# Kernel optimization log

Hardware: AMD Instinct MI355X
Metric: run time of the kernel (lower is better)

## Reference

```python
import jax, jax.numpy as jnp
import numpy as np

B, N, F = 4096, 64, 128   # batch, max_neighbor, input feature dim
H, D = 8, 64              # num_heads, weight_dims (per head)
HD = H * D


def setup_inputs() -> dict:
    key = jax.random.key(0)
    k1, k2, k3, k4 = jax.random.split(key, 4)
    x = jax.random.normal(k1, (B, N, F), dtype=jnp.float32)
    W_lin = jax.random.normal(k2, (F, HD), dtype=jnp.float32) * (1.0 / np.sqrt(F))
    W_att = jax.random.normal(k3, (2 * HD, H), dtype=jnp.float32) * (1.0 / np.sqrt(2 * HD))
    mask = jax.random.randint(k4, (B, N), 0, 2, dtype=jnp.int32)
    return {"x": x, "W_lin": W_lin, "W_att": W_att, "mask": mask}


def reference(x, W_lin, W_att, mask):
    # dropout is identity (rate 0.0 / inference)
    lin = x @ W_lin                               # [B, N, H*D]
    # src node is neighbor slot 0 of each batch row (the Python-loop gather+tile)
    src = lin[:, 0, :]                            # [B, H*D]
    # attention_layer on concat([src, lin]) == src@W_att[:HD] + lin@W_att[HD:]
    att = src @ W_att[:HD]                        # [B, H]
    att = att[:, None, :] + lin @ W_att[HD:]      # [B, N, H]
    att = jnp.where(att >= 0, att, 0.2 * att)     # LeakyReLU(alpha=0.2)
    aw = jnp.transpose(att, (0, 2, 1))            # [B, H, N]  (split heads + squeeze)
    aw = aw + (mask == 0).astype(jnp.float32)[:, None, :] * (-1e9)
    aw = jax.nn.softmax(aw, axis=2)[..., None]    # [B, H, N, 1]
    lp = jnp.transpose(lin.reshape(B, N, H, D), (0, 2, 1, 3))  # [B, H, N, D]
    weighted = lp * aw                            # [B, H, N, D]
    # fusion 'concat': unstack heads, concat along last -> [B, N, H*D], then ReLU
    out = jnp.transpose(weighted, (0, 2, 1, 3)).reshape(B, N, HD)
    return jax.nn.relu(out)
```

## Files before the change

kernel.cpp:

```cpp
#include <hip/hip_runtime.h>


typedef _Float16 half8  __attribute__((ext_vector_type(8)));
typedef _Float16 half4v __attribute__((ext_vector_type(4)));
typedef float    f32x4  __attribute__((ext_vector_type(4)));

static constexpr int NSEQ  = 64;
static constexpr int FIN   = 128;
static constexpr int HDIM  = 512;
static constexpr int NHEAD = 8;

static constexpr int ATT_OFF    = 34816;
static constexpr int SMEM_BYTES = 39168;

__global__ __launch_bounds__(256) void prep_kernel(const float* __restrict__ wlin,
                                                   const float* __restrict__ watt,
                                                   _Float16* __restrict__ wlinT,
                                                   _Float16* __restrict__ waA)
{
    int t = blockIdx.x * 256 + threadIdx.x;
    if (t < HDIM * FIN) {
        int c = t >> 7;
        int k = t & 127;
        wlinT[t] = (_Float16)wlin[k * HDIM + c];
    }
    if (t < 16 * HDIM) {
        int i     = t & 3;
        int lane  = (t >> 2) & 63;
        int slice = t >> 8;
        int c = (slice >> 2) * 64 + (slice & 3) * 16 + (lane >> 4) * 4 + i;
        int j = lane & 15;
        float v = (j < NHEAD) ? watt[(HDIM + c) * NHEAD + j]
                              : watt[c * NHEAD + (j - NHEAD)];
        waA[t] = (_Float16)v;
    }
}

__global__ __launch_bounds__(512, 4) void fused_kernel(const float* __restrict__ x,
                                                       const _Float16* __restrict__ wlinT,
                                                       const _Float16* __restrict__ waA,
                                                       const int* __restrict__ mask,
                                                       float* __restrict__ out)
{
    __shared__ char smem[SMEM_BYTES] __attribute__((aligned(16)));
    float* attbuf = (float*)smem;
    float* att_s  = (float*)(smem + ATT_OFF);

    const int b    = blockIdx.x;
    const int t    = threadIdx.x;
    const int lane = t & 63;
    const int w    = t >> 6;
    const int l15  = lane & 15;
    const int quad = lane >> 4;

    const int mv = mask[b * NSEQ + lane];

    f32x4 acc[4][4];
    #pragma unroll
    for (int mt = 0; mt < 4; ++mt)
        #pragma unroll
        for (int nt = 0; nt < 4; ++nt)
            acc[mt][nt] = (f32x4){0.f, 0.f, 0.f, 0.f};

    const float* xb = x + (size_t)b * (NSEQ * FIN);
    const int colbase = w * 64;
    #pragma unroll
    for (int ks = 0; ks < 4; ++ks) {
        const int k0 = ks * 32 + quad * 8;
        half8 a[4];
        #pragma unroll
        for (int mt = 0; mt < 4; ++mt)
            a[mt] = *(const half8*)(wlinT + (colbase + mt * 16 + l15) * FIN + k0);
        #pragma unroll
        for (int nt = 0; nt < 4; ++nt) {
            const float* xr = xb + (nt * 16 + l15) * FIN + k0;
            f32x4 v0 = *(const f32x4*)(xr);
            f32x4 v1 = *(const f32x4*)(xr + 4);
            half8 bfr;
            bfr[0] = (_Float16)v0[0]; bfr[1] = (_Float16)v0[1];
            bfr[2] = (_Float16)v0[2]; bfr[3] = (_Float16)v0[3];
            bfr[4] = (_Float16)v1[0]; bfr[5] = (_Float16)v1[1];
            bfr[6] = (_Float16)v1[2]; bfr[7] = (_Float16)v1[3];
            #pragma unroll
            for (int mt = 0; mt < 4; ++mt)
                acc[mt][nt] = __builtin_amdgcn_mfma_f32_16x16x32_f16(a[mt], bfr, acc[mt][nt], 0, 0, 0);
        }
    }

    {
        f32x4 T[4];
        #pragma unroll
        for (int nt = 0; nt < 4; ++nt) T[nt] = (f32x4){0.f, 0.f, 0.f, 0.f};
        #pragma unroll
        for (int mt = 0; mt < 4; ++mt) {
            half4v aF = *(const half4v*)(waA + ((w * 4 + mt) * 64 + lane) * 4);
            #pragma unroll
            for (int nt = 0; nt < 4; ++nt) {
                half4v bF;
                #pragma unroll
                for (int i = 0; i < 4; ++i) bF[i] = (_Float16)acc[mt][nt][i];
                T[nt] = __builtin_amdgcn_mfma_f32_16x16x16f16(aF, bF, T[nt], 0, 0, 0);
            }
        }
        #pragma unroll
        for (int nt = 0; nt < 4; ++nt)
            *(f32x4*)(attbuf + (w * 64 + nt * 16 + l15) * 16 + quad * 4) = T[nt];
    }
    __syncthreads();

    {
        int n  = t >> 3;
        int j0 = (t & 7) * 2;
        float s0 = 0.f, s1 = 0.f;
        #pragma unroll
        for (int ww = 0; ww < 8; ++ww) {
            const float* p = attbuf + (ww * 64 + n) * 16 + j0;
            s0 += p[0]; s1 += p[1];
        }
        att_s[n * 17 + j0]     = s0;
        att_s[n * 17 + j0 + 1] = s1;
    }
    __syncthreads();

    float aw_reg;
    {
        const float pen = (mv == 0) ? -1e9f : 0.0f;
        float a = att_s[lane * 17 + w] + att_s[8 + w];
        a = (a >= 0.0f) ? a : 0.2f * a;
        a += pen;
        float mx = a;
        #pragma unroll
        for (int off = 32; off > 0; off >>= 1)
            mx = fmaxf(mx, __shfl_xor(mx, off, 64));
        float e = __expf(a - mx);
        float s = e;
        #pragma unroll
        for (int off = 32; off > 0; off >>= 1)
            s += __shfl_xor(s, off, 64);
        aw_reg = e / s;
    }

    {
        float* ft = (float*)smem + w * (16 * 68);
        float* outb = out + (size_t)b * (NSEQ * HDIM);
        #pragma unroll
        for (int nt = 0; nt < 4; ++nt) {
            float awv = __shfl(aw_reg, nt * 16 + l15, 64);
            #pragma unroll
            for (int mt = 0; mt < 4; ++mt) {
                f32x4 o;
                #pragma unroll
                for (int i = 0; i < 4; ++i)
                    o[i] = fmaxf(acc[mt][nt][i] * awv, 0.0f);
                *(f32x4*)(ft + l15 * 68 + mt * 16 + quad * 4) = o;
            }
            #pragma unroll
            for (int s = 0; s < 4; ++s) {
                int r = s * 4 + quad;
                f32x4 v = *(const f32x4*)(ft + r * 68 + l15 * 4);
                int n = nt * 16 + r;
                __builtin_nontemporal_store(v, (f32x4*)(outb + n * HDIM + w * 64 + l15 * 4));
            }
        }
    }
}

extern "C" void kernel_launch(void* const* d_in, const int* in_sizes, int n_in,
                              void* d_out, int out_size, void* d_ws, size_t ws_size,
                              hipStream_t stream)
{
    const float* x    = (const float*)d_in[0];
    const float* wlin = (const float*)d_in[1];
    const float* watt = (const float*)d_in[2];
    const int*   mask = (const int*)d_in[3];
    float* out = (float*)d_out;

    _Float16* wlinT = (_Float16*)d_ws;
    _Float16* waA   = wlinT + HDIM * FIN;

    const int B = in_sizes[0] / (NSEQ * FIN);

    prep_kernel<<<256, 256, 0, stream>>>(wlin, watt, wlinT, waA);
    fused_kernel<<<B, 512, 0, stream>>>(x, wlinT, waA, mask, out);
}
```

Before: 746.2 us.

## Process four batches per block with double-buffered async x loads into LDS

Each block now handles four batch rows in sequence. While one row is computed, the next row's x tile is prefetched into a swizzled, double-buffered LDS region using global_load_lds. The cross-wave attention reduction changes from a staged buffer plus a second sync to LDS atomicAdd into a double-buffered accumulator. This aims to hide global load latency and remove one barrier per batch. In exchange LDS use grows to about 70KB per block, which reduces occupancy, and the grid shrinks by four times.

```diff
diff --git a/kernel.cpp b/kernel.cpp
--- a/kernel.cpp
+++ b/kernel.cpp
@@ -5,13 +5,24 @@
 typedef _Float16 half4v __attribute__((ext_vector_type(4)));
 typedef float    f32x4  __attribute__((ext_vector_type(4)));
 
-static constexpr int NSEQ  = 64;
-static constexpr int FIN   = 128;
-static constexpr int HDIM  = 512;
-static constexpr int NHEAD = 8;
-
-static constexpr int ATT_OFF    = 34816;
-static constexpr int SMEM_BYTES = 39168;
+static constexpr int NSEQ   = 64;
+static constexpr int FIN    = 128;
+static constexpr int HDIM   = 512;
+static constexpr int NHEAD  = 8;
+static constexpr int NBATCH = 4;
+static constexpr int AA_LD  = 17;
+
+static constexpr int XS_B       = 32768;
+static constexpr int FT7_OFF    = 65536;
+static constexpr int BLOB_BYTES = 69888;
+
+typedef const __attribute__((address_space(1))) unsigned int* gas_ptr;
+typedef __attribute__((address_space(3))) unsigned int*       las_ptr;
+
+__device__ __forceinline__ void gload_lds16(const void* g, void* l)
+{
+    __builtin_amdgcn_global_load_lds((gas_ptr)g, (las_ptr)l, 16, 0, 0);
+}
 
 __global__ __launch_bounds__(256) void prep_kernel(const float* __restrict__ wlin,
                                                    const float* __restrict__ watt,
@@ -42,126 +53,166 @@
                                                        const int* __restrict__ mask,
                                                        float* __restrict__ out)
 {
-    __shared__ char smem[SMEM_BYTES] __attribute__((aligned(16)));
-    float* attbuf = (float*)smem;
-    float* att_s  = (float*)(smem + ATT_OFF);
-
-    const int b    = blockIdx.x;
+    __shared__ char  smem[BLOB_BYTES] __attribute__((aligned(16)));
+    __shared__ float att_acc_s[2][NSEQ * AA_LD];
+
     const int t    = threadIdx.x;
     const int lane = t & 63;
     const int w    = t >> 6;
     const int l15  = lane & 15;
     const int quad = lane >> 4;
 
-    const int mv = mask[b * NSEQ + lane];
-
-    f32x4 acc[4][4];
-    #pragma unroll
-    for (int mt = 0; mt < 4; ++mt)
+    const int b0 = blockIdx.x * NBATCH;
+
+    {
+        int p0 = t, p1 = t + 512;
+        att_acc_s[0][(p0 >> 4) * AA_LD + (p0 & 15)] = 0.f;
+        att_acc_s[0][(p1 >> 4) * AA_LD + (p1 & 15)] = 0.f;
+        att_acc_s[1][(p0 >> 4) * AA_LD + (p0 & 15)] = 0.f;
+        att_acc_s[1][(p1 >> 4) * AA_LD + (p1 & 15)] = 0.f;
+    }
+
+    {
+        const char* xg = (const char*)(x + (size_t)b0 * (NSEQ * FIN));
         #pragma unroll
-        for (int nt = 0; nt < 4; ++nt)
-            acc[mt][nt] = (f32x4){0.f, 0.f, 0.f, 0.f};
-
-    const float* xb = x + (size_t)b * (NSEQ * FIN);
-    const int colbase = w * 64;
-    #pragma unroll
-    for (int ks = 0; ks < 4; ++ks) {
-        const int k0 = ks * 32 + quad * 8;
-        half8 a[4];
+        for (int j = 0; j < 4; ++j) {
+            int ci = j * 512 + t;
+            int L  = ci * 16;
+            int sw = ((ci >> 5) & 7) << 4;
+            gload_lds16(xg + (L ^ sw), smem + L);
+        }
+    }
+    __syncthreads();
+
+    #pragma unroll 1
+    for (int it = 0; it < NBATCH; ++it) {
+        const int b   = b0 + it;
+        const int cur = it & 1;
+        char*  xc = smem + cur * XS_B;
+        float* aa = att_acc_s[cur];
+
+        if (it + 1 < NBATCH) {
+            const char* xg = (const char*)(x + (size_t)(b + 1) * (NSEQ * FIN));
+            char* xn = smem + (cur ^ 1) * XS_B;
+            #pragma unroll
+            for (int j = 0; j < 4; ++j) {
+                int ci = j * 512 + t;
+                int L  = ci * 16;
+                int sw = ((ci >> 5) & 7) << 4;
+                gload_lds16(xg + (L ^ sw), xn + L);
+            }
+        }
+        const int mv = mask[b * NSEQ + lane];
+
+        f32x4 acc[4][4];
         #pragma unroll
         for (int mt = 0; mt < 4; ++mt)
-            a[mt] = *(const half8*)(wlinT + (colbase + mt * 16 + l15) * FIN + k0);
+            #pragma unroll
+            for (int nt = 0; nt < 4; ++nt)
+                acc[mt][nt] = (f32x4){0.f, 0.f, 0.f, 0.f};
+
+        const int colbase = w * 64;
         #pragma unroll
-        for (int nt = 0; nt < 4; ++nt) {
-            const float* xr = xb + (nt * 16 + l15) * FIN + k0;
-            f32x4 v0 = *(const f32x4*)(xr);
-            f32x4 v1 = *(const f32x4*)(xr + 4);
-            half8 bfr;
-            bfr[0] = (_Float16)v0[0]; bfr[1] = (_Float16)v0[1];
-            bfr[2] = (_Float16)v0[2]; bfr[3] = (_Float16)v0[3];
-            bfr[4] = (_Float16)v1[0]; bfr[5] = (_Float16)v1[1];
-            bfr[6] = (_Float16)v1[2]; bfr[7] = (_Float16)v1[3];
+        for (int ks = 0; ks < 4; ++ks) {
+            const int k0 = ks * 32 + quad * 8;
+            const int cb = k0 * 4;
+            half8 a[4];
             #pragma unroll
             for (int mt = 0; mt < 4; ++mt)
-                acc[mt][nt] = __builtin_amdgcn_mfma_f32_16x16x32_f16(a[mt], bfr, acc[mt][nt], 0, 0, 0);
-        }
-    }
-
-    {
-        f32x4 T[4];
-        #pragma unroll
-        for (int nt = 0; nt < 4; ++nt) T[nt] = (f32x4){0.f, 0.f, 0.f, 0.f};
-        #pragma unroll
-        for (int mt = 0; mt < 4; ++mt) {
-            half4v aF = *(const half4v*)(waA + ((w * 4 + mt) * 64 + lane) * 4);
+                a[mt] = *(const half8*)(wlinT + (colbase + mt * 16 + l15) * FIN + k0);
             #pragma unroll
             for (int nt = 0; nt < 4; ++nt) {
-                half4v bF;
-                #pragma unroll
-                for (int i = 0; i < 4; ++i) bF[i] = (_Float16)acc[mt][nt][i];
-                T[nt] = __builtin_amdgcn_mfma_f32_16x16x16f16(aF, bF, T[nt], 0, 0, 0);
-            }
-        }
-        #pragma unroll
-        for (int nt = 0; nt < 4; ++nt)
-            *(f32x4*)(attbuf + (w * 64 + nt * 16 + l15) * 16 + quad * 4) = T[nt];
-    }
-    __syncthreads();
-
-    {
-        int n  = t >> 3;
-        int j0 = (t & 7) * 2;
-        float s0 = 0.f, s1 = 0.f;
-        #pragma unroll
-        for (int ww = 0; ww < 8; ++ww) {
-            const float* p = attbuf + (ww * 64 + n) * 16 + j0;
-            s0 += p[0]; s1 += p[1];
-        }
-        att_s[n * 17 + j0]     = s0;
-        att_s[n * 17 + j0 + 1] = s1;
-    }
-    __syncthreads();
-
-    float aw_reg;
-    {
-        const float pen = (mv == 0) ? -1e9f : 0.0f;
-        float a = att_s[lane * 17 + w] + att_s[8 + w];
-        a = (a >= 0.0f) ? a : 0.2f * a;
-        a += pen;
-        float mx = a;
-        #pragma unroll
-        for (int off = 32; off > 0; off >>= 1)
-            mx = fmaxf(mx, __shfl_xor(mx, off, 64));
-        float e = __expf(a - mx);
-        float s = e;
-        #pragma unroll
-        for (int off = 32; off > 0; off >>= 1)
-            s += __shfl_xor(s, off, 64);
-        aw_reg = e / s;
-    }
-
-    {
-        float* ft = (float*)smem + w * (16 * 68);
-        float* outb = out + (size_t)b * (NSEQ * HDIM);
-        #pragma unroll
-        for (int nt = 0; nt < 4; ++nt) {
-            float awv = __shfl(aw_reg, nt * 16 + l15, 64);
+                const int n  = nt * 16 + l15;
+                const int sw = (n & 7) << 4;
+                const char* rb = xc + n * 512;
+                f32x4 v0 = *(const f32x4*)(rb + (cb ^ sw));
+                f32x4 v1 = *(const f32x4*)(rb + ((cb + 16) ^ sw));
+                half8 bfr;
+                bfr[0] = (_Float16)v0[0]; bfr[1] = (_Float16)v0[1];
+                bfr[2] = (_Float16)v0[2]; bfr[3] = (_Float16)v0[3];
+                bfr[4] = (_Float16)v1[0]; bfr[5] = (_Float16)v1[1];
+                bfr[6] = (_Float16)v1[2]; bfr[7] = (_Float16)v1[3];
+                #pragma unroll
+                for (int mt = 0; mt < 4; ++mt)
+                    acc[mt][nt] = __builtin_amdgcn_mfma_f32_16x16x32_f16(a[mt], bfr, acc[mt][nt], 0, 0, 0);
+            }
+        }
+
+        {
+            f32x4 T[4];
+            #pragma unroll
+            for (int nt = 0; nt < 4; ++nt) T[nt] = (f32x4){0.f, 0.f, 0.f, 0.f};
             #pragma unroll
             for (int mt = 0; mt < 4; ++mt) {
-                f32x4 o;
+                half4v aF = *(const half4v*)(waA + ((w * 4 + mt) * 64 + lane) * 4);
+                #pragma unroll
+                for (int nt = 0; nt < 4; ++nt) {
+                    half4v bF;
+                    #pragma unroll
+                    for (int i = 0; i < 4; ++i) bF[i] = (_Float16)acc[mt][nt][i];
+                    T[nt] = __builtin_amdgcn_mfma_f32_16x16x16f16(aF, bF, T[nt], 0, 0, 0);
+                }
+            }
+            #pragma unroll
+            for (int nt = 0; nt < 4; ++nt) {
+                const int n = nt * 16 + l15;
                 #pragma unroll
                 for (int i = 0; i < 4; ++i)
-                    o[i] = fmaxf(acc[mt][nt][i] * awv, 0.0f);
-                *(f32x4*)(ft + l15 * 68 + mt * 16 + quad * 4) = o;
-            }
-            #pragma unroll
-            for (int s = 0; s < 4; ++s) {
-                int r = s * 4 + quad;
-                f32x4 v = *(const f32x4*)(ft + r * 68 + l15 * 4);
-                int n = nt * 16 + r;
-                __builtin_nontemporal_store(v, (f32x4*)(outb + n * HDIM + w * 64 + l15 * 4));
-            }
-        }
+                    atomicAdd(&aa[n * AA_LD + quad * 4 + i], T[nt][i]);
+            }
+        }
+        __syncthreads();
+
+        {
+            float* ao = att_acc_s[cur ^ 1];
+            int p0 = t, p1 = t + 512;
+            ao[(p0 >> 4) * AA_LD + (p0 & 15)] = 0.f;
+            ao[(p1 >> 4) * AA_LD + (p1 & 15)] = 0.f;
+        }
+
+        float aw_reg;
+        {
+            const float pen = (mv == 0) ? -1e9f : 0.0f;
+            float a = aa[lane * AA_LD + w] + aa[8 + w];
+            a = (a >= 0.0f) ? a : 0.2f * a;
+            a += pen;
+            float mx = a;
+            #pragma unroll
+            for (int off = 32; off > 0; off >>= 1)
+                mx = fmaxf(mx, __shfl_xor(mx, off, 64));
+            float e = __expf(a - mx);
+            float s = e;
+            #pragma unroll
+            for (int off = 32; off > 0; off >>= 1)
+                s += __shfl_xor(s, off, 64);
+            aw_reg = e / s;
+        }
+
+        {
+            float* ft = (w < 7) ? (float*)xc + w * (16 * 68)
+                                : (float*)(smem + FT7_OFF);
+            float* outb = out + (size_t)b * (NSEQ * HDIM);
+            #pragma unroll
+            for (int nt = 0; nt < 4; ++nt) {
+                float awv = __shfl(aw_reg, nt * 16 + l15, 64);
+                #pragma unroll
+                for (int mt = 0; mt < 4; ++mt) {
+                    f32x4 o;
+                    #pragma unroll
+                    for (int i = 0; i < 4; ++i)
+                        o[i] = fmaxf(acc[mt][nt][i] * awv, 0.0f);
+                    *(f32x4*)(ft + l15 * 68 + mt * 16 + quad * 4) = o;
+                }
+                #pragma unroll
+                for (int s = 0; s < 4; ++s) {
+                    int r = s * 4 + quad;
+                    f32x4 v = *(const f32x4*)(ft + r * 68 + l15 * 4);
+                    int n = nt * 16 + r;
+                    __builtin_nontemporal_store(v, (f32x4*)(outb + n * HDIM + w * 64 + l15 * 4));
+                }
+            }
+        }
+        __syncthreads();
     }
 }
 
@@ -181,5 +232,5 @@
     const int B = in_sizes[0] / (NSEQ * FIN);
 
     prep_kernel<<<256, 256, 0, stream>>>(wlin, watt, wlinT, waA);
-    fused_kernel<<<B, 512, 0, stream>>>(x, wlinT, waA, mask, out);
-}
+    fused_kernel<<<B / NBATCH, 512, 0, stream>>>(x, wlinT, waA, mask, out);
+}
```

After: 835.0 us. 1.12x slower.
